# Kernel optimization log

Hardware: AMD Instinct MI355X
Metric: run time of the kernel (lower is better)

Reference implementation:

```python
import jax, jax.numpy as jnp
import numpy as np

N = 100000          # nodes
E = 3200000         # edges (avg degree 32)
F_IN = 512
NHID = 64
NCLS = 40
ALPHA = 0.1
K = 10

def setup_inputs() -> dict:
    key = jax.random.key(0)
    ks = jax.random.split(key, 6)
    features = jax.random.normal(ks[0], (N, F_IN), dtype=jnp.float32)
    edge_index = jax.random.randint(ks[1], (2, E), 0, N)
    edge_values = jax.random.uniform(ks[2], (E,), dtype=jnp.float32)
    W1 = jax.random.normal(ks[3], (F_IN, NHID), dtype=jnp.float32) * (1.0 / np.sqrt(F_IN))
    b1 = jnp.zeros((NHID,), jnp.float32)
    W2 = jax.random.normal(ks[4], (NHID, NCLS), dtype=jnp.float32) * (1.0 / np.sqrt(NHID))
    b2 = jnp.zeros((NCLS,), jnp.float32)
    return {"features": features, "edge_index": edge_index, "edge_values": edge_values,
            "W1": W1, "b1": b1, "W2": W2, "b2": b2}

def reference(features, edge_index, edge_values, W1, b1, W2, b2):
    # eval mode: all dropouts are identity
    row, col = edge_index[0], edge_index[1]
    x = jax.nn.relu(features @ W1 + b1)       # [N, NHID]
    x = x @ W2 + b2                            # [N, NCLS]
    h = x                                      # residual (teleport) term
    def step(x, _):
        msg = edge_values[:, None] * x[col]                       # [E, NCLS]
        agg = jax.ops.segment_sum(msg, row, num_segments=N)       # spmm(adj, x)
        return (1.0 - ALPHA) * agg + ALPHA * h, None
    x, _ = jax.lax.scan(step, x, None, length=K)
    return jax.nn.log_softmax(x, axis=1)
```

## Files before the change

### kernel.cpp

```cpp
#include <hip/hip_runtime.h>
#include <hip/hip_bf16.h>

#define NN 100000
#define NE 3200000
#define F_IN 512
#define NHID 64
#define NCLS 40

#define NB2 512
#define RPB2 196
#define CHK 4096
#define NCH 782
#define EPT 16
#define ECAP 7168
#define TOT (NB2 * NCH)
#define NSB 391

#define TPN 5

#define GCOL 64
#define CSH 11
#define NBIN (RPB2 * GCOL)
#define SEG (NBIN / 256)

__device__ __forceinline__ float bf2f(unsigned short u) {
  return __uint_as_float((unsigned)u << 16);
}
__device__ __forceinline__ unsigned short f2bf(float f) {
  unsigned u = __float_as_uint(f);
  u += 0x7FFFu + ((u >> 16) & 1u);
  return (unsigned short)(u >> 16);
}
__device__ __forceinline__ float blo(unsigned u) {
  return __uint_as_float(u << 16);
}
__device__ __forceinline__ float bhi(unsigned u) {
  return __uint_as_float(u & 0xffff0000u);
}
__device__ __forceinline__ unsigned pk(float l, float h) {
  return (unsigned)f2bf(l) | ((unsigned)f2bf(h) << 16);
}

__global__ __launch_bounds__(256) void gemm1_kernel(
    const float* __restrict__ F, const float* __restrict__ W1,
    const float* __restrict__ b1, float* __restrict__ H) {
  __shared__ float As[16][68];
  __shared__ float Bs[16][64];
  const int tid = threadIdx.x;
  const int m0 = blockIdx.x * 64;
  const int ty = tid >> 4;
  const int tx = tid & 15;
  const int lrowA = tid >> 2;
  const int lkA = (tid & 3) * 4;
  const int lkB = tid >> 4;
  const int lcolB = (tid & 15) * 4;
  const bool rowok = (m0 + lrowA) < NN;
  const int rclamp = rowok ? (m0 + lrowA) : (NN - 1);
  const float* Fb = F + (long)rclamp * F_IN + lkA;

  float acc[4][4] = {};
  for (int k0 = 0; k0 < F_IN; k0 += 16) {
    float4 fa = *(const float4*)(Fb + k0);
    if (!rowok) fa = make_float4(0.f, 0.f, 0.f, 0.f);
    float4 wb = *(const float4*)(W1 + (long)(k0 + lkB) * NHID + lcolB);
    __syncthreads();
    As[lkA + 0][lrowA] = fa.x;
    As[lkA + 1][lrowA] = fa.y;
    As[lkA + 2][lrowA] = fa.z;
    As[lkA + 3][lrowA] = fa.w;
    *(float4*)&Bs[lkB][lcolB] = wb;
    __syncthreads();
#pragma unroll
    for (int kk = 0; kk < 16; ++kk) {
      float4 a = *(const float4*)&As[kk][ty * 4];
      float4 b = *(const float4*)&Bs[kk][tx * 4];
      float av[4] = {a.x, a.y, a.z, a.w};
      float bv[4] = {b.x, b.y, b.z, b.w};
#pragma unroll
      for (int i = 0; i < 4; ++i)
#pragma unroll
        for (int j = 0; j < 4; ++j) acc[i][j] = fmaf(av[i], bv[j], acc[i][j]);
    }
  }
  float4 bb = *(const float4*)(b1 + tx * 4);
  float bv[4] = {bb.x, bb.y, bb.z, bb.w};
#pragma unroll
  for (int i = 0; i < 4; ++i) {
    int r = m0 + ty * 4 + i;
    if (r < NN) {
      float4 o;
      o.x = fmaxf(acc[i][0] + bv[0], 0.f);
      o.y = fmaxf(acc[i][1] + bv[1], 0.f);
      o.z = fmaxf(acc[i][2] + bv[2], 0.f);
      o.w = fmaxf(acc[i][3] + bv[3], 0.f);
      *(float4*)(H + (long)r * NHID + tx * 4) = o;
    }
  }
}

__global__ __launch_bounds__(256) void gemm2_kernel(
    const float* __restrict__ H, const float* __restrict__ W2,
    const float* __restrict__ b2, ushort4* __restrict__ X0b) {
  __shared__ float Ws[NHID * NCLS];
  __shared__ float bs[NCLS];
  const int tid = threadIdx.x;
  for (int i = tid; i < NHID * NCLS; i += 256) Ws[i] = W2[i];
  if (tid < NCLS) bs[tid] = b2[tid];
  __syncthreads();
  const int node = blockIdx.x * 256 + tid;
  if (node >= NN) return;
  float acc[NCLS];
#pragma unroll
  for (int j = 0; j < NCLS; ++j) acc[j] = bs[j];
  const float4* h4 = (const float4*)(H + (long)node * NHID);
#pragma unroll
  for (int kq = 0; kq < 16; ++kq) {
    float4 h = h4[kq];
    float hv[4] = {h.x, h.y, h.z, h.w};
#pragma unroll
    for (int u = 0; u < 4; ++u) {
      const int k = kq * 4 + u;
#pragma unroll
      for (int j = 0; j < NCLS; ++j)
        acc[j] = fmaf(hv[u], Ws[k * NCLS + j], acc[j]);
    }
  }
#pragma unroll
  for (int q = 0; q < 10; ++q) {
    X0b[node * 10 + q] = make_ushort4(f2bf(acc[q * 4]), f2bf(acc[q * 4 + 1]),
                                      f2bf(acc[q * 4 + 2]), f2bf(acc[q * 4 + 3]));
  }
}

__global__ __launch_bounds__(256) void p1_count(const int* __restrict__ row,
                                                int* __restrict__ hist) {
  __shared__ int h[NB2];
  const int tid = threadIdx.x, blk = blockIdx.x;
  for (int i = tid; i < NB2; i += 256) h[i] = 0;
  __syncthreads();
  const int e0 = blk * CHK;
#pragma unroll
  for (int k = 0; k < EPT; ++k) {
    int e = e0 + k * 256 + tid;
    if (e < NE) atomicAdd(&h[row[e] / RPB2], 1);
  }
  __syncthreads();
  for (int i = tid; i < NB2; i += 256) hist[blk * NB2 + i] = h[i];
}

__global__ __launch_bounds__(1024) void p2a_scan(const int* __restrict__ hist,
                                                 int* __restrict__ base,
                                                 int* __restrict__ bsum) {
  __shared__ int sm[1024];
  const int t = threadIdx.x;
  const int f = blockIdx.x * 1024 + t;
  const int b = f / NCH, blk = f - b * NCH;
  const int v = hist[blk * NB2 + b];
  sm[t] = v;
  __syncthreads();
  for (int off = 1; off < 1024; off <<= 1) {
    int u = (t >= off) ? sm[t - off] : 0;
    __syncthreads();
    sm[t] += u;
    __syncthreads();
  }
  base[f] = sm[t] - v;
  if (t == 1023) bsum[blockIdx.x] = sm[t];
}

__global__ __launch_bounds__(512) void p2b_scan(const int* __restrict__ bsum,
                                                int* __restrict__ boff) {
  __shared__ int sm[512];
  const int t = threadIdx.x;
  const int v = (t < NSB) ? bsum[t] : 0;
  sm[t] = v;
  __syncthreads();
  for (int off = 1; off < 512; off <<= 1) {
    int u = (t >= off) ? sm[t - off] : 0;
    __syncthreads();
    sm[t] += u;
    __syncthreads();
  }
  if (t < NSB) boff[t] = sm[t] - v;
}

__global__ __launch_bounds__(1024) void p2c_add(int* __restrict__ base,
                                                const int* __restrict__ boff) {
  const int f = blockIdx.x * 1024 + threadIdx.x;
  base[f] += boff[blockIdx.x];
}

__global__ __launch_bounds__(256) void p3_scatter(
    const int* __restrict__ row, const int* __restrict__ col,
    const float* __restrict__ ev, const int* __restrict__ base,
    int2* __restrict__ staged) {
  __shared__ int h[NB2], lscan[NB2], lcur[NB2], gbase[NB2];
  __shared__ int tmp[256];
  __shared__ int2 pay[CHK];
  __shared__ unsigned short binof[CHK];
  const int tid = threadIdx.x, blk = blockIdx.x;
  for (int i = tid; i < NB2; i += 256) { h[i] = 0; lcur[i] = 0; }
  __syncthreads();
  const int e0 = blk * CHK;
  const int n = (NE - e0 < CHK) ? (NE - e0) : CHK;
  int eb[EPT], em[EPT], ee[EPT];
#pragma unroll
  for (int k = 0; k < EPT; ++k) {
    int e = e0 + k * 256 + tid;
    if (e < NE) {
      int r = row[e];
      int b = r / RPB2;
      eb[k] = b;
      em[k] = (col[e] << 8) | (r - b * RPB2);
      ee[k] = __float_as_int(ev[e]);
      atomicAdd(&h[b], 1);
    } else {
      eb[k] = -1;
    }
  }
  __syncthreads();
  int a = h[2 * tid], c = h[2 * tid + 1];
  tmp[tid] = a + c;
  __syncthreads();
  for (int off = 1; off < 256; off <<= 1) {
    int v = (tid >= off) ? tmp[tid - off] : 0;
    __syncthreads();
    tmp[tid] += v;
    __syncthreads();
  }
  int excl = tmp[tid] - (a + c);
  lscan[2 * tid] = excl;
  lscan[2 * tid + 1] = excl + a;
  gbase[2 * tid] = base[(2 * tid) * NCH + blk];
  gbase[2 * tid + 1] = base[(2 * tid + 1) * NCH + blk];
  __syncthreads();
#pragma unroll
  for (int k = 0; k < EPT; ++k) {
    if (eb[k] >= 0) {
      int b = eb[k];
      int p = lscan[b] + atomicAdd(&lcur[b], 1);
      pay[p] = make_int2(em[k], ee[k]);
      binof[p] = (unsigned short)b;
    }
  }
  __syncthreads();
  for (int j = tid; j < n; j += 256) {
    int b = binof[j];
    staged[gbase[b] + (j - lscan[b])] = pay[j];
  }
}

__global__ __launch_bounds__(256) void p4_emit(
    const int* __restrict__ base, const int2* __restrict__ staged,
    int2* __restrict__ edges, int* __restrict__ rp) {
  __shared__ int bh[NBIN];
  __shared__ int tsum[256];
  __shared__ int2 pay[ECAP];
  const int b = blockIdx.x, tid = threadIdx.x;
  const int s0 = base[b * NCH];
  const int s1 = (b == NB2 - 1) ? NE : base[(b + 1) * NCH];
  const int cnt = s1 - s0;
  for (int i = tid; i < NBIN; i += 256) bh[i] = 0;
  __syncthreads();
  for (int j = tid; j < cnt; j += 256) {
    int ex = staged[s0 + j].x;
    int rl = ex & 255;
    unsigned col = (unsigned)ex >> 8;
    atomicAdd(&bh[(rl << 6) | (col >> CSH)], 1);
  }
  __syncthreads();
  int s = 0;
#pragma unroll
  for (int i = 0; i < SEG; ++i) {
    int v = bh[tid * SEG + i];
    bh[tid * SEG + i] = s;
    s += v;
  }
  tsum[tid] = s;
  __syncthreads();
  for (int off = 1; off < 256; off <<= 1) {
    int u = (tid >= off) ? tsum[tid - off] : 0;
    __syncthreads();
    tsum[tid] += u;
    __syncthreads();
  }
  const int add = (tid > 0) ? tsum[tid - 1] : 0;
#pragma unroll
  for (int i = 0; i < SEG; ++i) bh[tid * SEG + i] += add;
  __syncthreads();
  if (tid < RPB2) {
    int r = b * RPB2 + tid;
    if (r <= NN) rp[r] = s0 + bh[tid << 6];
  }
  __syncthreads();
  if (cnt <= ECAP) {
    for (int j = tid; j < cnt; j += 256) {
      int2 ed = staged[s0 + j];
      int rl = ed.x & 255;
      unsigned col = (unsigned)ed.x >> 8;
      int p = atomicAdd(&bh[(rl << 6) | (col >> CSH)], 1);
      pay[p] = make_int2((int)col, ed.y);
    }
    __syncthreads();
    for (int j = tid; j < cnt; j += 256) edges[s0 + j] = pay[j];
  } else {
    for (int j = tid; j < cnt; j += 256) {
      int2 ed = staged[s0 + j];
      int rl = ed.x & 255;
      unsigned col = (unsigned)ed.x >> 8;
      int p = atomicAdd(&bh[(rl << 6) | (col >> CSH)], 1);
      edges[s0 + p] = make_int2((int)col, ed.y);
    }
  }
}

#define FMA8(v, xb)                                              \
  a0 = fmaf(v, blo(xb.x), a0); a1 = fmaf(v, bhi(xb.x), a1);      \
  a2 = fmaf(v, blo(xb.y), a2); a3 = fmaf(v, bhi(xb.y), a3);      \
  a4 = fmaf(v, blo(xb.z), a4); a5 = fmaf(v, bhi(xb.z), a5);      \
  a6 = fmaf(v, blo(xb.w), a6); a7 = fmaf(v, bhi(xb.w), a7);

__global__ __launch_bounds__(256) void prop_kernel_bf16(
    const uint4* __restrict__ xin, uint4* __restrict__ xout,
    const uint4* __restrict__ hb, const int2* __restrict__ edges,
    const int* __restrict__ rp) {
  const int t = blockIdx.x * 256 + threadIdx.x;
  const int node = t / TPN;
  if (node >= NN) return;
  const int g = t - node * TPN;
  const int e0 = rp[node], e1 = rp[node + 1];
  float a0 = 0.f, a1 = 0.f, a2 = 0.f, a3 = 0.f;
  float a4 = 0.f, a5 = 0.f, a6 = 0.f, a7 = 0.f;
  int e = e0;
  if ((e & 1) && e < e1) {
    int2 ed = edges[e];
    float v = __int_as_float(ed.y);
    uint4 xb = xin[ed.x * TPN + g];
    FMA8(v, xb);
    ++e;
  }
  const int4* edges2 = (const int4*)edges;
  while (e + 2 <= e1) {
    int4 ep = edges2[e >> 1];
    float v0 = __int_as_float(ep.y);
    float v1 = __int_as_float(ep.w);
    uint4 xb0 = xin[ep.x * TPN + g];
    uint4 xb1 = xin[ep.z * TPN + g];
    FMA8(v0, xb0);
    FMA8(v1, xb1);
    e += 2;
  }
  if (e < e1) {
    int2 ed = edges[e];
    float v = __int_as_float(ed.y);
    uint4 xb = xin[ed.x * TPN + g];
    FMA8(v, xb);
  }
  uint4 hh = hb[node * TPN + g];
  uint4 r;
  r.x = pk(fmaf(0.9f, a0, 0.1f * blo(hh.x)), fmaf(0.9f, a1, 0.1f * bhi(hh.x)));
  r.y = pk(fmaf(0.9f, a2, 0.1f * blo(hh.y)), fmaf(0.9f, a3, 0.1f * bhi(hh.y)));
  r.z = pk(fmaf(0.9f, a4, 0.1f * blo(hh.z)), fmaf(0.9f, a5, 0.1f * bhi(hh.z)));
  r.w = pk(fmaf(0.9f, a6, 0.1f * blo(hh.w)), fmaf(0.9f, a7, 0.1f * bhi(hh.w)));
  xout[node * TPN + g] = r;
}

__global__ __launch_bounds__(256) void logsm_kernel(
    const ushort4* __restrict__ X, float* __restrict__ out) {
  const int node = blockIdx.x * 256 + threadIdx.x;
  if (node >= NN) return;
  float v[NCLS];
#pragma unroll
  for (int q = 0; q < 10; ++q) {
    ushort4 a = X[node * 10 + q];
    v[q * 4] = bf2f(a.x);
    v[q * 4 + 1] = bf2f(a.y);
    v[q * 4 + 2] = bf2f(a.z);
    v[q * 4 + 3] = bf2f(a.w);
  }
  float m = v[0];
#pragma unroll
  for (int j = 1; j < NCLS; ++j) m = fmaxf(m, v[j]);
  float s = 0.f;
#pragma unroll
  for (int j = 0; j < NCLS; ++j) s += expf(v[j] - m);
  const float l = m + logf(s);
  float4* o4 = (float4*)(out + (long)node * NCLS);
#pragma unroll
  for (int q = 0; q < 10; ++q)
    o4[q] = make_float4(v[q * 4] - l, v[q * 4 + 1] - l, v[q * 4 + 2] - l,
                        v[q * 4 + 3] - l);
}

extern "C" void kernel_launch(void* const* d_in, const int* in_sizes, int n_in,
                              void* d_out, int out_size, void* d_ws,
                              size_t ws_size, hipStream_t stream) {
  const float* F = (const float*)d_in[0];
  const int* EI = (const int*)d_in[1];
  const float* EV = (const float*)d_in[2];
  const float* W1 = (const float*)d_in[3];
  const float* b1 = (const float*)d_in[4];
  const float* W2 = (const float*)d_in[5];
  const float* b2 = (const float*)d_in[6];
  float* out = (float*)d_out;
  char* ws = (char*)d_ws;

  int2* STAGED = (int2*)(ws + 0);
  float* H = (float*)(ws + 16000000);
  int* HIST = (int*)(ws + 42000000);
  int* BASE = (int*)(ws + 43700000);
  int* BSUM = (int*)(ws + 45400000);
  int* BOFF = (int*)(ws + 45402048);
  int2* EDG = (int2*)(ws + 48000000);
  int* RP = (int*)(ws + 73600000);
  uint4* X0b = (uint4*)(ws + 76000000);
  uint4* XAb = (uint4*)(ws + 84000000);
  uint4* XBb = (uint4*)(ws + 92000000);

  const int* ROW = EI;
  const int* COL = EI + NE;

  p1_count<<<NCH, 256, 0, stream>>>(ROW, HIST);
  p2a_scan<<<NSB, 1024, 0, stream>>>(HIST, BASE, BSUM);
  p2b_scan<<<1, 512, 0, stream>>>(BSUM, BOFF);
  p2c_add<<<NSB, 1024, 0, stream>>>(BASE, BOFF);
  p3_scatter<<<NCH, 256, 0, stream>>>(ROW, COL, EV, BASE, STAGED);
  p4_emit<<<NB2, 256, 0, stream>>>(BASE, STAGED, EDG, RP);

  gemm1_kernel<<<(NN + 63) / 64, 256, 0, stream>>>(F, W1, b1, H);
  gemm2_kernel<<<(NN + 255) / 256, 256, 0, stream>>>(H, W2, b2,
                                                     (ushort4*)X0b);

  const int tgrid = (NN * TPN + 255) / 256;
  const uint4* cur_in = X0b;
  uint4* bufs[2] = {XAb, XBb};
  for (int it = 0; it < 10; ++it) {
    uint4* o = bufs[it & 1];
    prop_kernel_bf16<<<tgrid, 256, 0, stream>>>(cur_in, o, X0b, EDG, RP);
    cur_in = o;
  }
  logsm_kernel<<<(NN + 255) / 256, 256, 0, stream>>>((const ushort4*)cur_in,
                                                     out);
}
```

Baseline: 1.038 ms.

## Sort nodes by degree for propagation and unroll edge loop by four

Adds a counting sort of nodes by descending degree (histogram, scan, scatter) and has the propagation kernel process nodes in that permuted order, so the threads in a wavefront see similar edge counts and diverge less. The inner edge loop is also unrolled to four edges per iteration to keep more gathers in flight. In exchange it adds three small preprocessing kernels plus a memset, one extra indirection per node, and scattered row-pointer, h and output accesses, since neighbouring threads no longer touch neighbouring nodes.

```diff
diff --git a/kernel.cpp b/kernel.cpp
--- a/kernel.cpp
+++ b/kernel.cpp
@@ -22,6 +22,8 @@
 #define CSH 11
 #define NBIN (RPB2 * GCOL)
 #define SEG (NBIN / 256)
+
+#define DBIN 128
 
 __device__ __forceinline__ float bf2f(unsigned short u) {
   return __uint_as_float((unsigned)u << 16);
@@ -314,6 +316,50 @@
   }
 }
 
+__global__ __launch_bounds__(256) void d1_hist(const int* __restrict__ rp,
+                                               int* __restrict__ dh) {
+  __shared__ int h[DBIN];
+  const int tid = threadIdx.x;
+  if (tid < DBIN) h[tid] = 0;
+  __syncthreads();
+  const int n = blockIdx.x * 256 + tid;
+  if (n < NN) {
+    int d = rp[n + 1] - rp[n];
+    d = d > (DBIN - 1) ? (DBIN - 1) : d;
+    atomicAdd(&h[(DBIN - 1) - d], 1);
+  }
+  __syncthreads();
+  if (tid < DBIN && h[tid]) atomicAdd(&dh[tid], h[tid]);
+}
+
+__global__ __launch_bounds__(DBIN) void d2_scan(const int* __restrict__ dh,
+                                                int* __restrict__ doff) {
+  __shared__ int sm[DBIN];
+  const int t = threadIdx.x;
+  const int v = dh[t];
+  sm[t] = v;
+  __syncthreads();
+  for (int off = 1; off < DBIN; off <<= 1) {
+    int u = (t >= off) ? sm[t - off] : 0;
+    __syncthreads();
+    sm[t] += u;
+    __syncthreads();
+  }
+  doff[t] = sm[t] - v;
+}
+
+__global__ __launch_bounds__(256) void d3_scat(const int* __restrict__ rp,
+                                               int* __restrict__ doff,
+                                               int* __restrict__ perm) {
+  const int n = blockIdx.x * 256 + threadIdx.x;
+  if (n < NN) {
+    int d = rp[n + 1] - rp[n];
+    d = d > (DBIN - 1) ? (DBIN - 1) : d;
+    int p = atomicAdd(&doff[(DBIN - 1) - d], 1);
+    perm[p] = n;
+  }
+}
+
 #define FMA8(v, xb)                                              \
   a0 = fmaf(v, blo(xb.x), a0); a1 = fmaf(v, bhi(xb.x), a1);      \
   a2 = fmaf(v, blo(xb.y), a2); a3 = fmaf(v, bhi(xb.y), a3);      \
@@ -323,12 +369,13 @@
 __global__ __launch_bounds__(256) void prop_kernel_bf16(
     const uint4* __restrict__ xin, uint4* __restrict__ xout,
     const uint4* __restrict__ hb, const int2* __restrict__ edges,
-    const int* __restrict__ rp) {
+    const int* __restrict__ rp, const int* __restrict__ perm) {
   const int t = blockIdx.x * 256 + threadIdx.x;
-  const int node = t / TPN;
-  if (node >= NN) return;
-  const int g = t - node * TPN;
-  const int e0 = rp[node], e1 = rp[node + 1];
+  const int i = t / TPN;
+  if (i >= NN) return;
+  const int g = t - i * TPN;
+  const int nid = perm[i];
+  const int e0 = rp[nid], e1 = rp[nid + 1];
   float a0 = 0.f, a1 = 0.f, a2 = 0.f, a3 = 0.f;
   float a4 = 0.f, a5 = 0.f, a6 = 0.f, a7 = 0.f;
   int e = e0;
@@ -340,7 +387,24 @@
     ++e;
   }
   const int4* edges2 = (const int4*)edges;
-  while (e + 2 <= e1) {
+  while (e + 4 <= e1) {
+    int4 ea = edges2[e >> 1];
+    int4 eb = edges2[(e >> 1) + 1];
+    float v0 = __int_as_float(ea.y);
+    float v1 = __int_as_float(ea.w);
+    float v2 = __int_as_float(eb.y);
+    float v3 = __int_as_float(eb.w);
+    uint4 xb0 = xin[ea.x * TPN + g];
+    uint4 xb1 = xin[ea.z * TPN + g];
+    uint4 xb2 = xin[eb.x * TPN + g];
+    uint4 xb3 = xin[eb.z * TPN + g];
+    FMA8(v0, xb0);
+    FMA8(v1, xb1);
+    FMA8(v2, xb2);
+    FMA8(v3, xb3);
+    e += 4;
+  }
+  if (e + 2 <= e1) {
     int4 ep = edges2[e >> 1];
     float v0 = __int_as_float(ep.y);
     float v1 = __int_as_float(ep.w);
@@ -356,13 +420,13 @@
     uint4 xb = xin[ed.x * TPN + g];
     FMA8(v, xb);
   }
-  uint4 hh = hb[node * TPN + g];
+  uint4 hh = hb[nid * TPN + g];
   uint4 r;
   r.x = pk(fmaf(0.9f, a0, 0.1f * blo(hh.x)), fmaf(0.9f, a1, 0.1f * bhi(hh.x)));
   r.y = pk(fmaf(0.9f, a2, 0.1f * blo(hh.y)), fmaf(0.9f, a3, 0.1f * bhi(hh.y)));
   r.z = pk(fmaf(0.9f, a4, 0.1f * blo(hh.z)), fmaf(0.9f, a5, 0.1f * bhi(hh.z)));
   r.w = pk(fmaf(0.9f, a6, 0.1f * blo(hh.w)), fmaf(0.9f, a7, 0.1f * bhi(hh.w)));
-  xout[node * TPN + g] = r;
+  xout[nid * TPN + g] = r;
 }
 
 __global__ __launch_bounds__(256) void logsm_kernel(
@@ -413,6 +477,9 @@
   int* BOFF = (int*)(ws + 45402048);
   int2* EDG = (int2*)(ws + 48000000);
   int* RP = (int*)(ws + 73600000);
+  int* PERM = (int*)(ws + 74200000);
+  int* DHIST = (int*)(ws + 74800000);
+  int* DOFF = (int*)(ws + 74801024);
   uint4* X0b = (uint4*)(ws + 76000000);
   uint4* XAb = (uint4*)(ws + 84000000);
   uint4* XBb = (uint4*)(ws + 92000000);
@@ -427,6 +494,11 @@
   p3_scatter<<<NCH, 256, 0, stream>>>(ROW, COL, EV, BASE, STAGED);
   p4_emit<<<NB2, 256, 0, stream>>>(BASE, STAGED, EDG, RP);
 
+  hipMemsetAsync(DHIST, 0, DBIN * sizeof(int), stream);
+  d1_hist<<<(NN + 255) / 256, 256, 0, stream>>>(RP, DHIST);
+  d2_scan<<<1, DBIN, 0, stream>>>(DHIST, DOFF);
+  d3_scat<<<(NN + 255) / 256, 256, 0, stream>>>(RP, DOFF, PERM);
+
   gemm1_kernel<<<(NN + 63) / 64, 256, 0, stream>>>(F, W1, b1, H);
   gemm2_kernel<<<(NN + 255) / 256, 256, 0, stream>>>(H, W2, b2,
                                                      (ushort4*)X0b);
@@ -436,7 +508,7 @@
   uint4* bufs[2] = {XAb, XBb};
   for (int it = 0; it < 10; ++it) {
     uint4* o = bufs[it & 1];
-    prop_kernel_bf16<<<tgrid, 256, 0, stream>>>(cur_in, o, X0b, EDG, RP);
+    prop_kernel_bf16<<<tgrid, 256, 0, stream>>>(cur_in, o, X0b, EDG, RP, PERM);
     cur_in = o;
   }
   logsm_kernel<<<(NN + 255) / 256, 256, 0, stream>>>((const ushort4*)cur_in,
```

Result: slower. 1.188 ms (+14.5%).
